# Performance work log

Measured on AMD Instinct MI355X. Metric: run time of the kernel, lower is better.

The kernel has to match this reference:

```python
import jax, jax.numpy as jnp
import numpy as np
from jax import lax

B, C, H, W = 16, 128, 128, 128
WS, K = 2, 7
EPS = 1e-5


def setup_inputs() -> dict:
    key = jax.random.key(0)
    ks = jax.random.split(key, 4)
    s = 0.02
    return {
        "x": jax.random.normal(ks[0], (B, C, H, W), jnp.float32),
        "bn_gamma": jnp.ones((C,), jnp.float32),
        "bn_beta": jnp.zeros((C,), jnp.float32),
        "bn_mean": jnp.zeros((C,), jnp.float32),
        "bn_var": jnp.ones((C,), jnp.float32),
        "dw_w": jax.random.normal(ks[1], (C, 1, K, K), jnp.float32) * s,  # depthwise OIHW, groups=C
        "dw_b": jnp.zeros((C,), jnp.float32),
        "qkv_w": jax.random.normal(ks[2], (3 * C, C), jnp.float32) * s,  # 1x1 conv weight
        "qkv_b": jnp.zeros((3 * C,), jnp.float32),
        "proj_w": jax.random.normal(ks[3], (C, C), jnp.float32) * s,
        "proj_b": jnp.zeros((C,), jnp.float32),
    }


def reference(x, bn_gamma, bn_beta, bn_mean, bn_var, dw_w, dw_b, qkv_w, qkv_b, proj_w, proj_b):
    b, c, h, w = x.shape
    h2, w2 = h // WS, w // WS
    L = h2 * w2
    # --- ggm: BatchNorm (eval) -> GELU -> depthwise conv k=7 stride=2 pad=3 ---
    inv = lax.rsqrt(bn_var + EPS)
    xn = (x - bn_mean[None, :, None, None]) * (bn_gamma * inv)[None, :, None, None] + bn_beta[None, :, None, None]
    g = jax.nn.gelu(xn, approximate=False)
    guide = lax.conv_general_dilated(
        g, dw_w, window_strides=(WS, WS), padding=[(K // 2, K // 2), (K // 2, K // 2)],
        feature_group_count=c, dimension_numbers=("NCHW", "OIHW", "NCHW"),
    ) + dw_b[None, :, None, None]  # [B,C,H2,W2]
    # --- unfold(kernel=2, stride=2): non-overlapping 2x2 windows -> [B,C,4,L] ---
    xu = x.reshape(b, c, h2, WS, w2, WS).transpose(0, 1, 3, 5, 2, 4).reshape(b, c, WS * WS, L)
    tokens = jnp.concatenate([guide.reshape(b, c, 1, L), xu], axis=2)  # [B,C,5,L]
    # --- qkv 1x1 conv ---
    qkv = jnp.einsum("bcnl,dc->bdnl", tokens, qkv_w) + qkv_b[None, :, None, None]
    q, k, v = jnp.split(qkv, 3, axis=1)  # each [B,C,5,L]
    # --- tiny 5x5 attention per channel, contracting over the L window axis ---
    attn = jnp.einsum("bcnl,bcml->bcnm", q, k) / jnp.sqrt(jnp.float32(c))
    attn = jax.nn.softmax(attn, axis=-1)
    out = jnp.einsum("bcnm,bcml->bcnl", attn, v)  # [B,C,5,L]
    # take the guide-token row and fold back to the window grid
    out0 = out[:, :, 0, :].reshape(b, c, h2, w2)
    return jnp.einsum("bchw,dc->bdhw", out0, proj_w) + proj_b[None, :, None, None]
```

## Files before the change

kernel.cpp:

```cpp
#include <hip/hip_runtime.h>
#include <math.h>

#define BB 16
#define CC 128
#define HH 128
#define WW 128
#define LL 4096

typedef short short8 __attribute__((ext_vector_type(8)));
typedef float f32x4 __attribute__((ext_vector_type(4)));

__device__ __forceinline__ ushort f2bf(float f) {
    union { float f; unsigned u; } un; un.f = f;
    unsigned u = un.u;
    u += 0x7fffu + ((u >> 16) & 1u);
    return (ushort)(u >> 16);
}
__device__ __forceinline__ float bf2f(ushort h) {
    union { unsigned u; float f; } un; un.u = ((unsigned)h) << 16;
    return un.f;
}
__device__ __forceinline__ float fast_gelu(float xv) {
    float x2 = xv*xv;
    float arg = xv*(-2.3022100f - 0.1029436f*x2);
    float e = exp2f(arg);
    return xv*__builtin_amdgcn_rcpf(1.f + e);
}
__device__ __forceinline__ int swzkey(int r) { return (r & 3) ^ ((r >> 2) & 3); }

__global__ __launch_bounds__(128) void prep_cvec(
    const float* __restrict__ qkv_b, const float* __restrict__ proj_w,
    const float* __restrict__ proj_b, float* __restrict__ cvec)
{
    int t = threadIdx.x;
    float s = proj_b[t];
    const float* pr = proj_w + t*CC;
    const float* bv = qkv_b + 2*CC;
    for (int c = 0; c < CC; ++c) s += pr[c]*bv[c];
    cvec[t] = s;
}

__global__ __launch_bounds__(256) void guide_kernel(
    const float* __restrict__ x, const float* __restrict__ gamma,
    const float* __restrict__ beta, const float* __restrict__ mean,
    const float* __restrict__ var, const float* __restrict__ dww,
    const float* __restrict__ dwb, ushort* __restrict__ gw)
{
    int bc = blockIdx.x;
    int b = bc >> 7, c = bc & 127;
    int ty = blockIdx.y;
    __shared__ __align__(16) float g[69*144];
    int t = threadIdx.x;
    float wreg[49];
    #pragma unroll
    for (int k = 0; k < 49; ++k) wreg[k] = dww[c*49 + k];
    float bias = dwb[c];
    float scl = gamma[c] * rsqrtf(var[c] + 1e-5f);
    float sft = beta[c] - mean[c]*scl;
    const float* xb = x + (size_t)(b*CC + c)*HH*WW;
    int ihbase = 64*ty - 3;
    #pragma unroll
    for (int k = 0; k < 9; ++k) {
        int idx = k*256 + t;
        if (idx < 69*32) {
            int row = idx >> 5, ch = idx & 31;
            int ih = ihbase + row;
            float4 v4 = {0.f, 0.f, 0.f, 0.f};
            if ((unsigned)ih < 128u) {
                float4 xv = *(const float4*)(xb + ih*WW + 4*ch);
                v4.x = fast_gelu(xv.x*scl + sft);
                v4.y = fast_gelu(xv.y*scl + sft);
                v4.z = fast_gelu(xv.z*scl + sft);
                v4.w = fast_gelu(xv.w*scl + sft);
            }
            int f = (row >> 2) & 3;
            *(float4*)(g + row*144 + 4*((ch + 1) ^ f)) = v4;
        }
    }
    if (t < 138) {
        int row = t >> 1;
        int lc = (t & 1) ? 33 : 0;
        int f = (row >> 2) & 3;
        float4 z4 = {0.f, 0.f, 0.f, 0.f};
        *(float4*)(g + row*144 + 4*(lc ^ f)) = z4;
    }
    __syncthreads();
    int vg = t >> 4, owg = t & 15;
    float acc[2][4];
    #pragma unroll
    for (int v = 0; v < 2; ++v)
        #pragma unroll
        for (int hh = 0; hh < 4; ++hh) acc[v][hh] = bias;
    #pragma unroll
    for (int j = 0; j < 9; ++j) {
        int rr = 4*vg + j;
        int f = (rr >> 2) & 3;
        const float* grow = g + rr*144;
        float win[16];
        #pragma unroll
        for (int i = 0; i < 4; ++i) {
            float4 w4 = *(const float4*)(grow + 4*(((2*owg + i) ^ f)));
            win[4*i+0] = w4.x; win[4*i+1] = w4.y;
            win[4*i+2] = w4.z; win[4*i+3] = w4.w;
        }
        #pragma unroll
        for (int v = 0; v < 2; ++v) {
            int kh = j - 2*v;
            if (kh >= 0 && kh <= 6) {
                #pragma unroll
                for (int hh = 0; hh < 4; ++hh)
                    #pragma unroll
                    for (int kw = 0; kw < 7; ++kw)
                        acc[v][hh] += wreg[kh*7 + kw] * win[2*hh + kw + 1];
            }
        }
    }
    int orbase = 32*ty + 2*vg;
    ushort* gdst = gw + ((size_t)(b*CC + c) << 12);
    #pragma unroll
    for (int v = 0; v < 2; ++v) {
        uint2 pk;
        pk.x = (unsigned)f2bf(acc[v][0]) | ((unsigned)f2bf(acc[v][1]) << 16);
        pk.y = (unsigned)f2bf(acc[v][2]) | ((unsigned)f2bf(acc[v][3]) << 16);
        *(uint2*)(gdst + (orbase + v)*64 + 4*owg) = pk;
    }
}

__global__ __launch_bounds__(512) void gram_kernel(
    const float* __restrict__ x, const ushort* __restrict__ gw,
    float* __restrict__ Gpart, float* __restrict__ Tg, float* __restrict__ Txg)
{
    __shared__ __align__(16) ushort tokb[2*3*128*32];
    int t = threadIdx.x;
    int blk = blockIdx.x;
    int b = blk >> 5, kq = (blk >> 1) & 15, grp = blk & 1;
    int lane = t & 63, wid = t >> 6;
    int l15 = lane & 15, kg = lane >> 4;
    int js = t >> 2, sub = t & 3;
    int keyj = swzkey(js);
    const float* xrow0 = x + ((size_t)(b*CC + js)*HH + grp)*WW;
    const ushort* gwrow = gw + ((size_t)(b*CC + js) << 12);
    f32x4 acc[8][3];
    #pragma unroll
    for (int i = 0; i < 8; ++i)
        #pragma unroll
        for (int q = 0; q < 3; ++q) acc[i][q] = (f32x4){0.f,0.f,0.f,0.f};
    float tacc = 0.f, ps0 = 0.f, ps1 = 0.f;
    int H0 = kq*4;
    float4 xa, xbv, xc, xd;
    uint4 gr;
    {
        const float* xp = xrow0 + (2*H0)*WW + sub*16;
        xa = *(const float4*)(xp);
        xbv = *(const float4*)(xp + 4);
        xc = *(const float4*)(xp + 8);
        xd = *(const float4*)(xp + 12);
        gr = *(const uint4*)(gwrow + H0*64 + sub*8);
    }
    for (int s = 0; s < 8; ++s) {
        int cur = s & 1;
        ushort* tb = tokb + cur*(3*128*32);
        if (grp == 0) {
            tacc += bf2f((ushort)gr.x) + bf2f((ushort)(gr.x >> 16))
                  + bf2f((ushort)gr.y) + bf2f((ushort)(gr.y >> 16))
                  + bf2f((ushort)gr.z) + bf2f((ushort)(gr.z >> 16))
                  + bf2f((ushort)gr.w) + bf2f((ushort)(gr.w >> 16));
        }
        ps0 += xa.x + xa.z + xbv.x + xbv.z + xc.x + xc.z + xd.x + xd.z;
        ps1 += xa.y + xa.w + xbv.y + xbv.w + xc.y + xc.w + xd.y + xd.w;
        {
            unsigned lo0 = (unsigned)f2bf(xa.x) | ((unsigned)f2bf(xa.z) << 16);
            unsigned lo1 = (unsigned)f2bf(xbv.x) | ((unsigned)f2bf(xbv.z) << 16);
            unsigned lo2 = (unsigned)f2bf(xc.x) | ((unsigned)f2bf(xc.z) << 16);
            unsigned lo3 = (unsigned)f2bf(xd.x) | ((unsigned)f2bf(xd.z) << 16);
            unsigned hi0 = (unsigned)f2bf(xa.y) | ((unsigned)f2bf(xa.w) << 16);
            unsigned hi1 = (unsigned)f2bf(xbv.y) | ((unsigned)f2bf(xbv.w) << 16);
            unsigned hi2 = (unsigned)f2bf(xc.y) | ((unsigned)f2bf(xc.w) << 16);
            unsigned hi3 = (unsigned)f2bf(xd.y) | ((unsigned)f2bf(xd.w) << 16);
            uint4 lov = {lo0, lo1, lo2, lo3};
            uint4 hiv = {hi0, hi1, hi2, hi3};
            int chs = (sub ^ keyj) << 3;
            *(uint4*)(tb + (1*128 + js)*32 + chs) = lov;
            *(uint4*)(tb + (2*128 + js)*32 + chs) = hiv;
            *(uint4*)(tb + (0*128 + js)*32 + chs) = gr;
        }
        if (s < 7) {
            int sn = s + 1;
            int h = H0 + (sn >> 1), whalf = sn & 1;
            const float* xp = xrow0 + (2*h)*WW + whalf*64 + sub*16;
            xa = *(const float4*)(xp);
            xbv = *(const float4*)(xp + 4);
            xc = *(const float4*)(xp + 8);
            xd = *(const float4*)(xp + 12);
            gr = *(const uint4*)(gwrow + h*64 + whalf*32 + sub*8);
        }
        __syncthreads();
        const ushort* tb2 = tokb + cur*(3*128*32);
        short8 af[8];
        #pragma unroll
        for (int f = 0; f < 8; ++f) {
            int row = f*16 + l15;
            af[f] = *(const short8*)(tb2 + row*32 + ((kg ^ swzkey(row)) << 3));
        }
        if (grp == 0) {
            #pragma unroll
            for (int q = 0; q < 3; ++q) {
                int nf = wid*3 + q;
                int pl = nf >> 3, jr = (nf & 7)*16 + l15;
                short8 bf = *(const short8*)(tb2 + (pl*128 + jr)*32 + ((kg ^ swzkey(jr)) << 3));
                #pragma unroll
                for (int f = 0; f < 8; ++f)
                    acc[f][q] = __builtin_amdgcn_mfma_f32_16x16x32_bf16(af[f], bf, acc[f][q], 0, 0, 0);
            }
        } else {
            #pragma unroll
            for (int q = 0; q < 2; ++q) {
                int nf = wid*2 + q;
                int pl = 1 + (nf >> 3), jr = (nf & 7)*16 + l15;
                short8 bf = *(const short8*)(tb2 + (pl*128 + jr)*32 + ((kg ^ swzkey(jr)) << 3));
                #pragma unroll
                for (int f = 0; f < 8; ++f)
                    acc[f][q] = __builtin_amdgcn_mfma_f32_16x16x32_bf16(af[f], bf, acc[f][q], 0, 0, 0);
            }
        }
    }
    ps0 += __shfl_xor(ps0, 1); ps0 += __shfl_xor(ps0, 2);
    ps1 += __shfl_xor(ps1, 1); ps1 += __shfl_xor(ps1, 2);
    if (grp == 0) {
        tacc += __shfl_xor(tacc, 1); tacc += __shfl_xor(tacc, 2);
        if (sub == 0) Tg[(size_t)(b*16 + kq)*128 + js] = tacc;
    }
    if (sub == 0) {
        float* tx = Txg + (((size_t)(b*16 + kq)*2 + grp)*2)*128;
        tx[js] = ps0;
        tx[128 + js] = ps1;
    }
    float* gp = Gpart + (size_t)(b*16 + kq)*81920;
    if (grp == 0) {
        #pragma unroll
        for (int f = 0; f < 8; ++f)
            #pragma unroll
            for (int q = 0; q < 3; ++q) {
                int n = (wid*3 + q)*16 + l15;
                #pragma unroll
                for (int r = 0; r < 4; ++r)
                    gp[(size_t)(f*16 + kg*4 + r)*640 + n] = acc[f][q][r];
            }
    } else {
        #pragma unroll
        for (int f = 0; f < 8; ++f)
            #pragma unroll
            for (int q = 0; q < 2; ++q) {
                int n = 384 + (wid*2 + q)*16 + l15;
                #pragma unroll
                for (int r = 0; r < 4; ++r)
                    gp[(size_t)(f*16 + kg*4 + r)*640 + n] = acc[f][q][r];
            }
    }
}

__global__ __launch_bounds__(256) void combine_kernel(
    const float* __restrict__ Gpart, const float* __restrict__ Tg,
    const float* __restrict__ Txg, const float* __restrict__ qkv_w,
    const float* __restrict__ qkv_b, float* __restrict__ Sout)
{
    __shared__ float Gm[128*129];
    __shared__ float Wks[128*129];
    __shared__ float Ts[5*128];
    int blk = blockIdx.x;
    int b = blk / 5, m = blk % 5;
    int t = threadIdx.x;
    for (int idx4 = t; idx4 < 4096; idx4 += 256) {
        int i = idx4 >> 5, j4 = idx4 & 31;
        float4 ws = {0.f,0.f,0.f,0.f};
        #pragma unroll
        for (int kq = 0; kq < 16; ++kq) {
            float4 v = *(const float4*)(Gpart + (size_t)(b*16+kq)*81920
                                        + (size_t)i*640 + m*128 + j4*4);
            ws.x += v.x; ws.y += v.y; ws.z += v.z; ws.w += v.w;
        }
        Gm[i*129 + j4*4 + 0] = ws.x;
        Gm[i*129 + j4*4 + 1] = ws.y;
        Gm[i*129 + j4*4 + 2] = ws.z;
        Gm[i*129 + j4*4 + 3] = ws.w;
        float4 wk = *(const float4*)(qkv_w + (size_t)(128 + i)*128 + j4*4);
        Wks[i*129 + j4*4 + 0] = wk.x;
        Wks[i*129 + j4*4 + 1] = wk.y;
        Wks[i*129 + j4*4 + 2] = wk.z;
        Wks[i*129 + j4*4 + 3] = wk.w;
    }
    for (int i2 = t; i2 < 640; i2 += 256) {
        int v = i2 >> 7, c = i2 & 127;
        float s = 0.f;
        if (v == 0) {
            for (int p = 0; p < 16; ++p) s += Tg[(size_t)(b*16 + p)*128 + c];
        } else {
            int grp = (v - 1) >> 1, pi = (v - 1) & 1;
            for (int p = 0; p < 16; ++p)
                s += Txg[(((size_t)(b*16 + p)*2 + grp)*2 + pi)*128 + c];
        }
        Ts[v*128 + c] = s;
    }
    __syncthreads();
    int ti = t >> 4, tc = t & 15;
    float au[8][8];
    #pragma unroll
    for (int r = 0; r < 8; ++r)
        #pragma unroll
        for (int s2 = 0; s2 < 8; ++s2) au[r][s2] = 0.f;
    for (int j = 0; j < 128; ++j) {
        float gmr[8], wkr[8];
        #pragma unroll
        for (int r = 0; r < 8; ++r) gmr[r] = Gm[(ti*8 + r)*129 + j];
        #pragma unroll
        for (int s2 = 0; s2 < 8; ++s2) wkr[s2] = Wks[(tc*8 + s2)*129 + j];
        #pragma unroll
        for (int r = 0; r < 8; ++r)
            #pragma unroll
            for (int s2 = 0; s2 < 8; ++s2) au[r][s2] += gmr[r]*wkr[s2];
    }
    __syncthreads();
    #pragma unroll
    for (int r = 0; r < 8; ++r)
        #pragma unroll
        for (int s2 = 0; s2 < 8; ++s2)
            Gm[(ti*8 + r)*129 + tc*8 + s2] = au[r][s2];
    __syncthreads();
    if (t < 128) {
        int c = t;
        const float4* wq4p = (const float4*)(qkv_w + (size_t)c*128);
        float bq = qkv_b[c], bk = qkv_b[128 + c];
        float ud = 0.f, t0d = 0.f, km = 0.f;
        for (int k4 = 0; k4 < 32; ++k4) {
            float4 w4 = wq4p[k4];
            int k = k4*4;
            ud  += w4.x*Gm[(k+0)*129 + c] + w4.y*Gm[(k+1)*129 + c]
                 + w4.z*Gm[(k+2)*129 + c] + w4.w*Gm[(k+3)*129 + c];
            t0d += w4.x*Ts[k+0] + w4.y*Ts[k+1] + w4.z*Ts[k+2] + w4.w*Ts[k+3];
            km  += Wks[c*129 + k+0]*Ts[m*128 + k+0] + Wks[c*129 + k+1]*Ts[m*128 + k+1]
                 + Wks[c*129 + k+2]*Ts[m*128 + k+2] + Wks[c*129 + k+3]*Ts[m*128 + k+3];
        }
        Sout[(size_t)(b*128 + c)*5 + m] = ud + bq*km + bk*t0d + 4096.0f*bq*bk;
    }
}

__global__ __launch_bounds__(128) void softmax_attn(
    const float* __restrict__ Sout, float* __restrict__ attn)
{
    int b = blockIdx.x, c = threadIdx.x;
    const float* sp = Sout + (size_t)(b*128 + c)*5;
    const float scale = 0.08838834764831845f;
    float s[5];
    #pragma unroll
    for (int m = 0; m < 5; ++m) s[m] = sp[m]*scale;
    float mx = s[0];
    #pragma unroll
    for (int m = 1; m < 5; ++m) mx = fmaxf(mx, s[m]);
    float e[5], tot = 0.f;
    #pragma unroll
    for (int m = 0; m < 5; ++m) { e[m] = expf(s[m] - mx); tot += e[m]; }
    float inv = 1.f/tot;
    #pragma unroll
    for (int m = 0; m < 5; ++m) attn[(size_t)(b*128 + c)*5 + m] = e[m]*inv;
}

__global__ __launch_bounds__(256) void pw_kernel(
    const float* __restrict__ qkv_w, const float* __restrict__ proj_w,
    const float* __restrict__ attn, ushort* __restrict__ PW)
{
    __shared__ float attns[CC];
    __shared__ float wvs[32*CC];
    int blk = blockIdx.x;
    int b = blk / 5, m = blk % 5;
    int t = threadIdx.x;
    if (t < CC) attns[t] = attn[(b*CC + t)*5 + m];
    int d = t >> 1, cb = (t & 1)*64;
    float acc[64];
    #pragma unroll
    for (int j = 0; j < 64; ++j) acc[j] = 0.f;
    for (int cc0 = 0; cc0 < CC; cc0 += 32) {
        __syncthreads();
        for (int idx = t; idx < 32*CC; idx += 256) {
            int row = idx >> 7, col = idx & 127;
            wvs[idx] = qkv_w[(2*CC + cc0 + row)*CC + col];
        }
        __syncthreads();
        for (int cl = 0; cl < 32; ++cl) {
            int c = cc0 + cl;
            float a = proj_w[d*CC + c]*attns[c];
            const float* wr = wvs + cl*CC + cb;
            #pragma unroll
            for (int j = 0; j < 64; ++j) acc[j] += a*wr[j];
        }
    }
    ushort* dst = PW + ((size_t)(b*5 + m) << 14) + d*CC + cb;
    #pragma unroll
    for (int j = 0; j < 64; ++j) dst[j] = f2bf(acc[j]);
}

__global__ __launch_bounds__(256) void y_kernel(
    const float* __restrict__ x, const ushort* __restrict__ gw,
    const ushort* __restrict__ PW, const float* __restrict__ cvec,
    float* __restrict__ out)
{
    __shared__ __align__(16) ushort tok[5*32*128];
    int t = threadIdx.x;
    int blk = blockIdx.x;
    int b = blk >> 7, chunk = blk & 127;
    int h = chunk >> 1, whalf = chunk & 1;
    int lane = t & 63, wave = t >> 6;
    int l15 = lane & 15, kg = lane >> 4;
    int swz = (l15 & 7) << 3;
    int c = t >> 1, r = t & 1;
    const ushort* gsrc = gw + ((size_t)(b*CC + c) << 12) + h*64 + whalf*32 + r*16;
    uint4 g0 = *(const uint4*)gsrc;
    uint4 g1 = *(const uint4*)(gsrc + 8);
    const float* xrow = x + ((size_t)(b*CC + c)*HH + 2*h + r)*WW + whalf*64;
    float4 xv[16];
    #pragma unroll
    for (int i = 0; i < 16; ++i) xv[i] = ((const float4*)xrow)[i];
    {
        unsigned wd[8] = {g0.x,g0.y,g0.z,g0.w,g1.x,g1.y,g1.z,g1.w};
        #pragma unroll
        for (int k2 = 0; k2 < 8; ++k2) {
            int lp0 = r*16 + 2*k2, lp1 = lp0 + 1;
            tok[lp0*128 + (c ^ ((lp0 & 7) << 3))] = (ushort)wd[k2];
            tok[lp1*128 + (c ^ ((lp1 & 7) << 3))] = (ushort)(wd[k2] >> 16);
        }
    }
    {
        int mA = (1 + 2*r)*4096, mB = (2 + 2*r)*4096;
        #pragma unroll
        for (int i = 0; i < 16; ++i) {
            int lp0 = 2*i, lp1 = 2*i + 1;
            int o0 = lp0*128 + (c ^ ((lp0 & 7) << 3));
            int o1 = lp1*128 + (c ^ ((lp1 & 7) << 3));
            tok[mA + o0] = f2bf(xv[i].x);
            tok[mB + o0] = f2bf(xv[i].y);
            tok[mA + o1] = f2bf(xv[i].z);
            tok[mB + o1] = f2bf(xv[i].w);
        }
    }
    __syncthreads();
    f32x4 acc[2][2] = {};
    #pragma unroll
    for (int m = 0; m < 5; ++m) {
        const ushort* pwb = PW + ((size_t)(b*5 + m) << 14)
                          + ((wave*32 + l15) << 7) + (kg << 3);
        #pragma unroll
        for (int kt = 0; kt < 4; ++kt) {
            int ko = (kt*32 + kg*8) ^ swz;
            short8 a0 = *(const short8*)(tok + m*4096 + (l15     )*128 + ko);
            short8 a1 = *(const short8*)(tok + m*4096 + (16 + l15)*128 + ko);
            short8 b0 = *(const short8*)(pwb + kt*32);
            short8 b1 = *(const short8*)(pwb + (16 << 7) + kt*32);
            acc[0][0] = __builtin_amdgcn_mfma_f32_16x16x32_bf16(a0, b0, acc[0][0], 0, 0, 0);
            acc[0][1] = __builtin_amdgcn_mfma_f32_16x16x32_bf16(a0, b1, acc[0][1], 0, 0, 0);
            acc[1][0] = __builtin_amdgcn_mfma_f32_16x16x32_bf16(a1, b0, acc[1][0], 0, 0, 0);
            acc[1][1] = __builtin_amdgcn_mfma_f32_16x16x32_bf16(a1, b1, acc[1][1], 0, 0, 0);
        }
    }
    __syncthreads();
    float* ylds = (float*)tok;
    #pragma unroll
    for (int mt = 0; mt < 2; ++mt)
        #pragma unroll
        for (int ntl = 0; ntl < 2; ++ntl) {
            int cc = wave*32 + ntl*16 + l15;
            float cv = cvec[cc];
            #pragma unroll
            for (int rr = 0; rr < 4; ++rr) {
                int l = mt*16 + kg*4 + rr;
                ylds[cc*36 + l] = acc[mt][ntl][rr] + cv;
            }
        }
    __syncthreads();
    int c2 = t >> 1, half = t & 1;
    float* ob = out + ((size_t)(b*CC + c2) << 12) + h*64 + whalf*32 + half*16;
    const float* yr = ylds + c2*36 + half*16;
    #pragma unroll
    for (int j = 0; j < 4; ++j)
        ((float4*)ob)[j] = ((const float4*)yr)[j];
}

extern "C" void kernel_launch(void* const* d_in, const int* in_sizes, int n_in,
                              void* d_out, int out_size, void* d_ws, size_t ws_size,
                              hipStream_t stream) {
    const float* x        = (const float*)d_in[0];
    const float* bn_gamma = (const float*)d_in[1];
    const float* bn_beta  = (const float*)d_in[2];
    const float* bn_mean  = (const float*)d_in[3];
    const float* bn_var   = (const float*)d_in[4];
    const float* dw_w     = (const float*)d_in[5];
    const float* dw_b     = (const float*)d_in[6];
    const float* qkv_w    = (const float*)d_in[7];
    const float* qkv_b    = (const float*)d_in[8];
    const float* proj_w   = (const float*)d_in[9];
    const float* proj_b   = (const float*)d_in[10];
    float* out = (float*)d_out;

    char* w = (char*)d_ws;
    ushort* gw    = (ushort*)w; w += (size_t)BB*CC*LL*2;
    ushort* PW    = (ushort*)w; w += (size_t)BB*5*CC*CC*2;
    float*  Gpart = (float*)w;  w += (size_t)BB*16*81920*4;
    float*  Tg    = (float*)w;  w += (size_t)BB*16*128*4;
    float*  Txg   = (float*)w;  w += (size_t)BB*16*2*2*128*4;
    float*  Sout  = (float*)w;  w += (size_t)BB*CC*5*4;
    float*  attn  = (float*)w;  w += (size_t)BB*CC*5*4;
    float*  cvec  = (float*)w;  w += (size_t)CC*4;

    prep_cvec<<<1, 128, 0, stream>>>(qkv_b, proj_w, proj_b, cvec);
    guide_kernel<<<dim3(BB*CC, 2), 256, 0, stream>>>(
        x, bn_gamma, bn_beta, bn_mean, bn_var, dw_w, dw_b, gw);
    gram_kernel<<<512, 512, 0, stream>>>(x, gw, Gpart, Tg, Txg);
    combine_kernel<<<80, 256, 0, stream>>>(Gpart, Tg, Txg, qkv_w, qkv_b, Sout);
    softmax_attn<<<BB, 128, 0, stream>>>(Sout, attn);
    pw_kernel<<<BB*5, 256, 0, stream>>>(qkv_w, proj_w, attn, PW);
    y_kernel<<<2048, 256, 0, stream>>>(x, gw, PW, cvec, out);
}
```

Measured before the change: 240.5 us.

## Cache bf16 copy of x in guide pass; split combine across more blocks

```diff
diff --git a/kernel.cpp b/kernel.cpp
--- a/kernel.cpp
+++ b/kernel.cpp
@@ -44,7 +44,8 @@
     const float* __restrict__ x, const float* __restrict__ gamma,
     const float* __restrict__ beta, const float* __restrict__ mean,
     const float* __restrict__ var, const float* __restrict__ dww,
-    const float* __restrict__ dwb, ushort* __restrict__ gw)
+    const float* __restrict__ dwb, ushort* __restrict__ gw,
+    ushort* __restrict__ xbf)
 {
     int bc = blockIdx.x;
     int b = bc >> 7, c = bc & 127;
@@ -58,6 +59,7 @@
     float scl = gamma[c] * rsqrtf(var[c] + 1e-5f);
     float sft = beta[c] - mean[c]*scl;
     const float* xb = x + (size_t)(b*CC + c)*HH*WW;
+    ushort* xbb = xbf + (((size_t)(b*CC + c)) << 14);
     int ihbase = 64*ty - 3;
     #pragma unroll
     for (int k = 0; k < 9; ++k) {
@@ -68,6 +70,12 @@
             float4 v4 = {0.f, 0.f, 0.f, 0.f};
             if ((unsigned)ih < 128u) {
                 float4 xv = *(const float4*)(xb + ih*WW + 4*ch);
+                if (row >= 3 && row < 67) {
+                    uint2 pk2;
+                    pk2.x = (unsigned)f2bf(xv.x) | ((unsigned)f2bf(xv.y) << 16);
+                    pk2.y = (unsigned)f2bf(xv.z) | ((unsigned)f2bf(xv.w) << 16);
+                    *(uint2*)(xbb + (ih << 7) + 4*ch) = pk2;
+                }
                 v4.x = fast_gelu(xv.x*scl + sft);
                 v4.y = fast_gelu(xv.y*scl + sft);
                 v4.z = fast_gelu(xv.z*scl + sft);
@@ -127,7 +135,7 @@
 }
 
 __global__ __launch_bounds__(512) void gram_kernel(
-    const float* __restrict__ x, const ushort* __restrict__ gw,
+    const ushort* __restrict__ xbf, const ushort* __restrict__ gw,
     float* __restrict__ Gpart, float* __restrict__ Tg, float* __restrict__ Txg)
 {
     __shared__ __align__(16) ushort tokb[2*3*128*32];
@@ -138,7 +146,7 @@
     int l15 = lane & 15, kg = lane >> 4;
     int js = t >> 2, sub = t & 3;
     int keyj = swzkey(js);
-    const float* xrow0 = x + ((size_t)(b*CC + js)*HH + grp)*WW;
+    const ushort* xrow0 = xbf + ((((size_t)(b*CC + js))*HH + grp) << 7);
     const ushort* gwrow = gw + ((size_t)(b*CC + js) << 12);
     f32x4 acc[8][3];
     #pragma unroll
@@ -147,14 +155,11 @@
         for (int q = 0; q < 3; ++q) acc[i][q] = (f32x4){0.f,0.f,0.f,0.f};
     float tacc = 0.f, ps0 = 0.f, ps1 = 0.f;
     int H0 = kq*4;
-    float4 xa, xbv, xc, xd;
-    uint4 gr;
+    uint4 xd0, xd1, gr;
     {
-        const float* xp = xrow0 + (2*H0)*WW + sub*16;
-        xa = *(const float4*)(xp);
-        xbv = *(const float4*)(xp + 4);
-        xc = *(const float4*)(xp + 8);
-        xd = *(const float4*)(xp + 12);
+        const ushort* xp = xrow0 + ((2*H0) << 7) + sub*16;
+        xd0 = *(const uint4*)xp;
+        xd1 = *(const uint4*)(xp + 8);
         gr = *(const uint4*)(gwrow + H0*64 + sub*8);
     }
     for (int s = 0; s < 8; ++s) {
@@ -166,17 +171,19 @@
                   + bf2f((ushort)gr.z) + bf2f((ushort)(gr.z >> 16))
                   + bf2f((ushort)gr.w) + bf2f((ushort)(gr.w >> 16));
         }
-        ps0 += xa.x + xa.z + xbv.x + xbv.z + xc.x + xc.z + xd.x + xd.z;
-        ps1 += xa.y + xa.w + xbv.y + xbv.w + xc.y + xc.w + xd.y + xd.w;
         {
-            unsigned lo0 = (unsigned)f2bf(xa.x) | ((unsigned)f2bf(xa.z) << 16);
-            unsigned lo1 = (unsigned)f2bf(xbv.x) | ((unsigned)f2bf(xbv.z) << 16);
-            unsigned lo2 = (unsigned)f2bf(xc.x) | ((unsigned)f2bf(xc.z) << 16);
-            unsigned lo3 = (unsigned)f2bf(xd.x) | ((unsigned)f2bf(xd.z) << 16);
-            unsigned hi0 = (unsigned)f2bf(xa.y) | ((unsigned)f2bf(xa.w) << 16);
-            unsigned hi1 = (unsigned)f2bf(xbv.y) | ((unsigned)f2bf(xbv.w) << 16);
-            unsigned hi2 = (unsigned)f2bf(xc.y) | ((unsigned)f2bf(xc.w) << 16);
-            unsigned hi3 = (unsigned)f2bf(xd.y) | ((unsigned)f2bf(xd.w) << 16);
+            unsigned lo0 = (xd0.x & 0xffffu) | (xd0.y << 16);
+            unsigned hi0 = (xd0.x >> 16)     | (xd0.y & 0xffff0000u);
+            unsigned lo1 = (xd0.z & 0xffffu) | (xd0.w << 16);
+            unsigned hi1 = (xd0.z >> 16)     | (xd0.w & 0xffff0000u);
+            unsigned lo2 = (xd1.x & 0xffffu) | (xd1.y << 16);
+            unsigned hi2 = (xd1.x >> 16)     | (xd1.y & 0xffff0000u);
+            unsigned lo3 = (xd1.z & 0xffffu) | (xd1.w << 16);
+            unsigned hi3 = (xd1.z >> 16)     | (xd1.w & 0xffff0000u);
+            ps0 += bf2f((ushort)lo0)+bf2f((ushort)(lo0>>16))+bf2f((ushort)lo1)+bf2f((ushort)(lo1>>16))
+                 + bf2f((ushort)lo2)+bf2f((ushort)(lo2>>16))+bf2f((ushort)lo3)+bf2f((ushort)(lo3>>16));
+            ps1 += bf2f((ushort)hi0)+bf2f((ushort)(hi0>>16))+bf2f((ushort)hi1)+bf2f((ushort)(hi1>>16))
+                 + bf2f((ushort)hi2)+bf2f((ushort)(hi2>>16))+bf2f((ushort)hi3)+bf2f((ushort)(hi3>>16));
             uint4 lov = {lo0, lo1, lo2, lo3};
             uint4 hiv = {hi0, hi1, hi2, hi3};
             int chs = (sub ^ keyj) << 3;
@@ -187,11 +194,9 @@
         if (s < 7) {
             int sn = s + 1;
             int h = H0 + (sn >> 1), whalf = sn & 1;
-            const float* xp = xrow0 + (2*h)*WW + whalf*64 + sub*16;
-            xa = *(const float4*)(xp);
-            xbv = *(const float4*)(xp + 4);
-            xc = *(const float4*)(xp + 8);
-            xd = *(const float4*)(xp + 12);
+            const ushort* xp = xrow0 + ((2*h) << 7) + whalf*64 + sub*16;
+            xd0 = *(const uint4*)xp;
+            xd1 = *(const uint4*)(xp + 8);
             gr = *(const uint4*)(gwrow + h*64 + whalf*32 + sub*8);
         }
         __syncthreads();
@@ -259,106 +264,92 @@
     }
 }
 
-__global__ __launch_bounds__(256) void combine_kernel(
-    const float* __restrict__ Gpart, const float* __restrict__ Tg,
+__global__ __launch_bounds__(256) void combine2_kernel(
+    const float* __restrict__ Gpart, const float* __restrict__ qkv_w,
+    float* __restrict__ Spart2)
+{
+    __shared__ float Gm[32*128];
+    int blk = blockIdx.x;
+    int iq = blk & 3, bm = blk >> 2;
+    int b = bm / 5, m = bm - b*5;
+    int t = threadIdx.x;
+    int i0 = iq*32;
+    for (int e = t; e < 32*128; e += 256) {
+        int i = e >> 7, j = e & 127;
+        float s = 0.f;
+        #pragma unroll
+        for (int kq = 0; kq < 16; ++kq)
+            s += Gpart[(size_t)(b*16 + kq)*81920 + (size_t)(i0 + i)*640 + m*128 + j];
+        Gm[e] = s;
+    }
+    __syncthreads();
+    int c = t >> 1, jh = t & 1;
+    float wkr[64];
+    const float* wkp = qkv_w + (size_t)(128 + c)*128 + jh*64;
+    #pragma unroll
+    for (int q = 0; q < 16; ++q)
+        *(float4*)&wkr[q*4] = ((const float4*)wkp)[q];
+    const float* wqp = qkv_w + (size_t)c*128 + i0;
+    float acc = 0.f;
+    for (int i = 0; i < 32; ++i) {
+        const float4* gr4 = (const float4*)(Gm + i*128 + jh*64);
+        float val = 0.f;
+        #pragma unroll
+        for (int q = 0; q < 16; ++q) {
+            float4 g4 = gr4[q];
+            val += wkr[q*4+0]*g4.x + wkr[q*4+1]*g4.y
+                 + wkr[q*4+2]*g4.z + wkr[q*4+3]*g4.w;
+        }
+        acc += wqp[i]*val;
+    }
+    acc += __shfl_xor(acc, 1);
+    if (jh == 0) Spart2[((size_t)bm*4 + iq)*128 + c] = acc;
+}
+
+__global__ __launch_bounds__(128) void softmax_attn(
+    const float* __restrict__ Spart2, const float* __restrict__ Tg,
     const float* __restrict__ Txg, const float* __restrict__ qkv_w,
-    const float* __restrict__ qkv_b, float* __restrict__ Sout)
-{
-    __shared__ float Gm[128*129];
-    __shared__ float Wks[128*129];
+    const float* __restrict__ qkv_b, float* __restrict__ attn)
+{
     __shared__ float Ts[5*128];
-    int blk = blockIdx.x;
-    int b = blk / 5, m = blk % 5;
-    int t = threadIdx.x;
-    for (int idx4 = t; idx4 < 4096; idx4 += 256) {
-        int i = idx4 >> 5, j4 = idx4 & 31;
-        float4 ws = {0.f,0.f,0.f,0.f};
-        #pragma unroll
-        for (int kq = 0; kq < 16; ++kq) {
-            float4 v = *(const float4*)(Gpart + (size_t)(b*16+kq)*81920
-                                        + (size_t)i*640 + m*128 + j4*4);
-            ws.x += v.x; ws.y += v.y; ws.z += v.z; ws.w += v.w;
-        }
-        Gm[i*129 + j4*4 + 0] = ws.x;
-        Gm[i*129 + j4*4 + 1] = ws.y;
-        Gm[i*129 + j4*4 + 2] = ws.z;
-        Gm[i*129 + j4*4 + 3] = ws.w;
-        float4 wk = *(const float4*)(qkv_w + (size_t)(128 + i)*128 + j4*4);
-        Wks[i*129 + j4*4 + 0] = wk.x;
-        Wks[i*129 + j4*4 + 1] = wk.y;
-        Wks[i*129 + j4*4 + 2] = wk.z;
-        Wks[i*129 + j4*4 + 3] = wk.w;
-    }
-    for (int i2 = t; i2 < 640; i2 += 256) {
-        int v = i2 >> 7, c = i2 & 127;
+    int b = blockIdx.x, t = threadIdx.x;
+    #pragma unroll
+    for (int v = 0; v < 5; ++v) {
         float s = 0.f;
         if (v == 0) {
-            for (int p = 0; p < 16; ++p) s += Tg[(size_t)(b*16 + p)*128 + c];
+            for (int p = 0; p < 16; ++p) s += Tg[(size_t)(b*16 + p)*128 + t];
         } else {
             int grp = (v - 1) >> 1, pi = (v - 1) & 1;
             for (int p = 0; p < 16; ++p)
-                s += Txg[(((size_t)(b*16 + p)*2 + grp)*2 + pi)*128 + c];
-        }
-        Ts[v*128 + c] = s;
+                s += Txg[(((size_t)(b*16 + p)*2 + grp)*2 + pi)*128 + t];
+        }
+        Ts[v*128 + t] = s;
     }
     __syncthreads();
-    int ti = t >> 4, tc = t & 15;
-    float au[8][8];
-    #pragma unroll
-    for (int r = 0; r < 8; ++r)
-        #pragma unroll
-        for (int s2 = 0; s2 < 8; ++s2) au[r][s2] = 0.f;
-    for (int j = 0; j < 128; ++j) {
-        float gmr[8], wkr[8];
-        #pragma unroll
-        for (int r = 0; r < 8; ++r) gmr[r] = Gm[(ti*8 + r)*129 + j];
-        #pragma unroll
-        for (int s2 = 0; s2 < 8; ++s2) wkr[s2] = Wks[(tc*8 + s2)*129 + j];
-        #pragma unroll
-        for (int r = 0; r < 8; ++r)
-            #pragma unroll
-            for (int s2 = 0; s2 < 8; ++s2) au[r][s2] += gmr[r]*wkr[s2];
-    }
-    __syncthreads();
-    #pragma unroll
-    for (int r = 0; r < 8; ++r)
-        #pragma unroll
-        for (int s2 = 0; s2 < 8; ++s2)
-            Gm[(ti*8 + r)*129 + tc*8 + s2] = au[r][s2];
-    __syncthreads();
-    if (t < 128) {
-        int c = t;
-        const float4* wq4p = (const float4*)(qkv_w + (size_t)c*128);
-        float bq = qkv_b[c], bk = qkv_b[128 + c];
-        float ud = 0.f, t0d = 0.f, km = 0.f;
-        for (int k4 = 0; k4 < 32; ++k4) {
-            float4 w4 = wq4p[k4];
-            int k = k4*4;
-            ud  += w4.x*Gm[(k+0)*129 + c] + w4.y*Gm[(k+1)*129 + c]
-                 + w4.z*Gm[(k+2)*129 + c] + w4.w*Gm[(k+3)*129 + c];
-            t0d += w4.x*Ts[k+0] + w4.y*Ts[k+1] + w4.z*Ts[k+2] + w4.w*Ts[k+3];
-            km  += Wks[c*129 + k+0]*Ts[m*128 + k+0] + Wks[c*129 + k+1]*Ts[m*128 + k+1]
-                 + Wks[c*129 + k+2]*Ts[m*128 + k+2] + Wks[c*129 + k+3]*Ts[m*128 + k+3];
-        }
-        Sout[(size_t)(b*128 + c)*5 + m] = ud + bq*km + bk*t0d + 4096.0f*bq*bk;
-    }
-}
-
-__global__ __launch_bounds__(128) void softmax_attn(
-    const float* __restrict__ Sout, float* __restrict__ attn)
-{
-    int b = blockIdx.x, c = threadIdx.x;
-    const float* sp = Sout + (size_t)(b*128 + c)*5;
+    int c = t;
+    float bq = qkv_b[c], bk = qkv_b[128 + c];
+    const float* wqr = qkv_w + (size_t)c*128;
+    const float* wkr = qkv_w + (size_t)(128 + c)*128;
+    float t0d = 0.f;
+    for (int j = 0; j < 128; ++j) t0d += wqr[j]*Ts[j];
+    float s5[5];
+    #pragma unroll
+    for (int m = 0; m < 5; ++m) {
+        float km = 0.f;
+        for (int j = 0; j < 128; ++j) km += wkr[j]*Ts[m*128 + j];
+        float ss = 0.f;
+        #pragma unroll
+        for (int iq = 0; iq < 4; ++iq)
+            ss += Spart2[((size_t)(b*5 + m)*4 + iq)*128 + c];
+        s5[m] = ss + bq*km + bk*t0d + 4096.0f*bq*bk;
+    }
     const float scale = 0.08838834764831845f;
-    float s[5];
-    #pragma unroll
-    for (int m = 0; m < 5; ++m) s[m] = sp[m]*scale;
-    float mx = s[0];
-    #pragma unroll
-    for (int m = 1; m < 5; ++m) mx = fmaxf(mx, s[m]);
+    float mx = s5[0]*scale;
+    #pragma unroll
+    for (int m = 1; m < 5; ++m) mx = fmaxf(mx, s5[m]*scale);
     float e[5], tot = 0.f;
     #pragma unroll
-    for (int m = 0; m < 5; ++m) { e[m] = expf(s[m] - mx); tot += e[m]; }
+    for (int m = 0; m < 5; ++m) { e[m] = expf(s5[m]*scale - mx); tot += e[m]; }
     float inv = 1.f/tot;
     #pragma unroll
     for (int m = 0; m < 5; ++m) attn[(size_t)(b*128 + c)*5 + m] = e[m]*inv;
@@ -399,7 +390,7 @@
 }
 
 __global__ __launch_bounds__(256) void y_kernel(
-    const float* __restrict__ x, const ushort* __restrict__ gw,
+    const ushort* __restrict__ xbf, const ushort* __restrict__ gw,
     const ushort* __restrict__ PW, const float* __restrict__ cvec,
     float* __restrict__ out)
 {
@@ -415,10 +406,10 @@
     const ushort* gsrc = gw + ((size_t)(b*CC + c) << 12) + h*64 + whalf*32 + r*16;
     uint4 g0 = *(const uint4*)gsrc;
     uint4 g1 = *(const uint4*)(gsrc + 8);
-    const float* xrow = x + ((size_t)(b*CC + c)*HH + 2*h + r)*WW + whalf*64;
-    float4 xv[16];
-    #pragma unroll
-    for (int i = 0; i < 16; ++i) xv[i] = ((const float4*)xrow)[i];
+    const ushort* xrow = xbf + ((((size_t)(b*CC + c))*HH + 2*h + r) << 7) + whalf*64;
+    uint4 xq[8];
+    #pragma unroll
+    for (int i = 0; i < 8; ++i) xq[i] = ((const uint4*)xrow)[i];
     {
         unsigned wd[8] = {g0.x,g0.y,g0.z,g0.w,g1.x,g1.y,g1.z,g1.w};
         #pragma unroll
@@ -431,14 +422,16 @@
     {
         int mA = (1 + 2*r)*4096, mB = (2 + 2*r)*4096;
         #pragma unroll
-        for (int i = 0; i < 16; ++i) {
-            int lp0 = 2*i, lp1 = 2*i + 1;
-            int o0 = lp0*128 + (c ^ ((lp0 & 7) << 3));
-            int o1 = lp1*128 + (c ^ ((lp1 & 7) << 3));
-            tok[mA + o0] = f2bf(xv[i].x);
-            tok[mB + o0] = f2bf(xv[i].y);
-            tok[mA + o1] = f2bf(xv[i].z);
-            tok[mB + o1] = f2bf(xv[i].w);
+        for (int i = 0; i < 8; ++i) {
+            unsigned d0 = xq[i].x, d1 = xq[i].y, d2 = xq[i].z, d3 = xq[i].w;
+            unsigned dd[4] = {d0, d1, d2, d3};
+            #pragma unroll
+            for (int j = 0; j < 4; ++j) {
+                int lp = 4*i + j;
+                int o = lp*128 + (c ^ ((lp & 7) << 3));
+                tok[mA + o] = (ushort)dd[j];
+                tok[mB + o] = (ushort)(dd[j] >> 16);
+            }
         }
     }
     __syncthreads();
@@ -500,21 +493,22 @@
     float* out = (float*)d_out;
 
     char* w = (char*)d_ws;
-    ushort* gw    = (ushort*)w; w += (size_t)BB*CC*LL*2;
-    ushort* PW    = (ushort*)w; w += (size_t)BB*5*CC*CC*2;
-    float*  Gpart = (float*)w;  w += (size_t)BB*16*81920*4;
-    float*  Tg    = (float*)w;  w += (size_t)BB*16*128*4;
-    float*  Txg   = (float*)w;  w += (size_t)BB*16*2*2*128*4;
-    float*  Sout  = (float*)w;  w += (size_t)BB*CC*5*4;
-    float*  attn  = (float*)w;  w += (size_t)BB*CC*5*4;
-    float*  cvec  = (float*)w;  w += (size_t)CC*4;
+    ushort* gw     = (ushort*)w; w += (size_t)BB*CC*LL*2;
+    ushort* xbf    = (ushort*)w; w += (size_t)BB*CC*HH*WW*2;
+    ushort* PW     = (ushort*)w; w += (size_t)BB*5*CC*CC*2;
+    float*  Gpart  = (float*)w;  w += (size_t)BB*16*81920*4;
+    float*  Tg     = (float*)w;  w += (size_t)BB*16*128*4;
+    float*  Txg    = (float*)w;  w += (size_t)BB*16*2*2*128*4;
+    float*  Spart2 = (float*)w;  w += (size_t)BB*5*4*128*4;
+    float*  attn   = (float*)w;  w += (size_t)BB*CC*5*4;
+    float*  cvec   = (float*)w;  w += (size_t)CC*4;
 
     prep_cvec<<<1, 128, 0, stream>>>(qkv_b, proj_w, proj_b, cvec);
     guide_kernel<<<dim3(BB*CC, 2), 256, 0, stream>>>(
-        x, bn_gamma, bn_beta, bn_mean, bn_var, dw_w, dw_b, gw);
-    gram_kernel<<<512, 512, 0, stream>>>(x, gw, Gpart, Tg, Txg);
-    combine_kernel<<<80, 256, 0, stream>>>(Gpart, Tg, Txg, qkv_w, qkv_b, Sout);
-    softmax_attn<<<BB, 128, 0, stream>>>(Sout, attn);
+        x, bn_gamma, bn_beta, bn_mean, bn_var, dw_w, dw_b, gw, xbf);
+    gram_kernel<<<512, 512, 0, stream>>>(xbf, gw, Gpart, Tg, Txg);
+    combine2_kernel<<<BB*5*4, 256, 0, stream>>>(Gpart, qkv_w, Spart2);
+    softmax_attn<<<BB, 128, 0, stream>>>(Spart2, Tg, Txg, qkv_w, qkv_b, attn);
     pw_kernel<<<BB*5, 256, 0, stream>>>(qkv_w, proj_w, attn, PW);
-    y_kernel<<<2048, 256, 0, stream>>>(x, gw, PW, cvec, out);
-}
+    y_kernel<<<2048, 256, 0, stream>>>(xbf, gw, PW, cvec, out);
+}
```

Result: slower. 273.6 us (+13.8%).
